# Kernel tuning notes

Hardware: AMD Instinct MI355X
Metric: run time of the kernel (lower is better)

Reference implementation:

```python
import jax, jax.numpy as jnp
import numpy as np

N = 50000          # num nodes
EPS = 1e-5         # BatchNorm eps


def _spmm(row, col, val, x):
    # sparse (COO) @ dense: out[r] += val_e * x[c] for each edge e=(r,c)
    return jax.ops.segment_sum(val[:, None] * x[col], row, num_segments=N)


def setup_inputs() -> dict:
    key = jax.random.key(0)
    ks = jax.random.split(key, 12)
    E1, E2 = 1_000_000, 2_000_000
    IN, H, OUT = 512, 64, 40
    return {
        "x": jax.random.normal(ks[0], (N, IN), jnp.float32),
        "adj_row": jax.random.randint(ks[1], (E1,), 0, N, jnp.int32),
        "adj_col": jax.random.randint(ks[2], (E1,), 0, N, jnp.int32),
        "adj_val": jax.random.uniform(ks[3], (E1,), jnp.float32),
        "adj2_row": jax.random.randint(ks[4], (E2,), 0, N, jnp.int32),
        "adj2_col": jax.random.randint(ks[5], (E2,), 0, N, jnp.int32),
        "adj2_val": jax.random.uniform(ks[6], (E2,), jnp.float32),
        "W_embed": jax.random.normal(ks[7], (IN, H), jnp.float32) * 0.05,
        "b_embed": jnp.zeros((H,), jnp.float32),
        "bn_gamma": jnp.ones((2 * H,), jnp.float32),
        "bn_beta": jnp.zeros((2 * H,), jnp.float32),
        "bn_mean": jax.random.normal(ks[8], (2 * H,), jnp.float32) * 0.1,
        "bn_var": jax.random.uniform(ks[9], (2 * H,), jnp.float32) + 0.5,
        "W_final": jax.random.normal(ks[10], (7 * H, OUT), jnp.float32) * 0.05,
        "b_final": jnp.zeros((OUT,), jnp.float32),
    }


def reference(x, adj_row, adj_col, adj_val, adj2_row, adj2_col, adj2_val,
              W_embed, b_embed, bn_gamma, bn_beta, bn_mean, bn_var,
              W_final, b_final):
    # feature embed (1-layer MLP) + relu
    h = jax.nn.relu(x @ W_embed + b_embed)                       # [N, H]
    xs = [h]
    # conv 1: two-hop aggregation + concat, then BatchNorm (eval mode)
    h1 = jnp.concatenate([_spmm(adj_row, adj_col, adj_val, h),
                          _spmm(adj2_row, adj2_col, adj2_val, h)], axis=1)  # [N, 2H]
    h1 = (h1 - bn_mean) * jax.lax.rsqrt(bn_var + EPS) * bn_gamma + bn_beta
    xs.append(h1)
    # conv 2 (last conv, no BN)
    h2 = jnp.concatenate([_spmm(adj_row, adj_col, adj_val, h1),
                          _spmm(adj2_row, adj2_col, adj2_val, h1)], axis=1)  # [N, 4H]
    xs.append(h2)
    # JumpingKnowledge cat -> [N, 7H], final projection
    jk = jnp.concatenate(xs, axis=1)
    return jk @ W_final + b_final                                # [N, OUT]
```

## Files before the change

kernel.cpp:

```cpp
#include <hip/hip_runtime.h>

#define BN_EPS 1e-5f
#define MAXBINS 128

typedef __attribute__((ext_vector_type(8))) short bf16x8;
typedef __attribute__((ext_vector_type(4))) float f32x4;

__device__ __forceinline__ ushort f2bf(float f) {
  uint u = __float_as_uint(f);
  u += 0x7fffu + ((u >> 16) & 1u);
  return (ushort)(u >> 16);
}
__device__ __forceinline__ float bf2f(ushort u) {
  return __uint_as_float((uint)u << 16);
}
__device__ __forceinline__ uint pack2bf(float a, float b) {
  return (uint)f2bf(a) | ((uint)f2bf(b) << 16);
}
__device__ __forceinline__ void fma8(float acc[8], uint4 wv, float v) {
  acc[0] += v * __uint_as_float(wv.x << 16);
  acc[1] += v * __uint_as_float(wv.x & 0xffff0000u);
  acc[2] += v * __uint_as_float(wv.y << 16);
  acc[3] += v * __uint_as_float(wv.y & 0xffff0000u);
  acc[4] += v * __uint_as_float(wv.z << 16);
  acc[5] += v * __uint_as_float(wv.z & 0xffff0000u);
  acc[6] += v * __uint_as_float(wv.w << 16);
  acc[7] += v * __uint_as_float(wv.w & 0xffff0000u);
}

__global__ __launch_bounds__(256) void prep_weights(
    const float* __restrict__ We, const float* __restrict__ Wf,
    ushort* __restrict__ Wet, ushort* __restrict__ Wtg) {
  int i = blockIdx.x * 256 + threadIdx.x;
  if (i < 32768) {
    int col = i >> 9, k = i & 511;
    Wet[(size_t)col * 512 + k] = f2bf(We[(size_t)k * 64 + col]);
  } else if (i < 32768 + 24576) {
    int j = i - 32768;
    int col = j / 192, k = j % 192;
    float v = 0.f;
    if (col < 40)       v = Wf[(size_t)k * 40 + col];
    else if (col < 80)  { if (k >= 64) v = Wf[(size_t)(128 + k) * 40 + (col - 40)]; }
    else if (col < 120) { if (k >= 64) v = Wf[(size_t)(256 + k) * 40 + (col - 80)]; }
    Wtg[(size_t)col * 192 + k] = f2bf(v);
  }
}

__global__ __launch_bounds__(256) void embed_mfma(
    const float* __restrict__ x, const ushort* __restrict__ Wet,
    const float* __restrict__ b, ushort* __restrict__ hb, int N) {
  const int tid  = threadIdx.x;
  const int wv   = tid >> 6;
  const int lane = tid & 63;
  const int m16  = lane & 15;
  const int kg   = lane >> 4;
  const int row0 = blockIdx.x * 128 + wv * 32;

  f32x4 acc[2][4];
#pragma unroll
  for (int i = 0; i < 2; ++i)
#pragma unroll
    for (int t = 0; t < 4; ++t) acc[i][t] = (f32x4){0.f, 0.f, 0.f, 0.f};

#pragma unroll 4
  for (int ks = 0; ks < 16; ++ks) {
    const int kk = ks * 32 + kg * 8;
    bf16x8 afr[2];
#pragma unroll
    for (int i = 0; i < 2; ++i) {
      int grow = row0 + i * 16 + m16;
      grow = (grow < N) ? grow : (N - 1);
      const float* ap = x + (size_t)grow * 512 + kk;
      float4 lo = *reinterpret_cast<const float4*>(ap);
      float4 hi = *reinterpret_cast<const float4*>(ap + 4);
      uint4 pk;
      pk.x = pack2bf(lo.x, lo.y); pk.y = pack2bf(lo.z, lo.w);
      pk.z = pack2bf(hi.x, hi.y); pk.w = pack2bf(hi.z, hi.w);
      afr[i] = *reinterpret_cast<const bf16x8*>(&pk);
    }
#pragma unroll
    for (int t = 0; t < 4; ++t) {
      bf16x8 bfr = *reinterpret_cast<const bf16x8*>(
          Wet + (size_t)(t * 16 + m16) * 512 + kk);
      acc[0][t] = __builtin_amdgcn_mfma_f32_16x16x32_bf16(afr[0], bfr, acc[0][t], 0, 0, 0);
      acc[1][t] = __builtin_amdgcn_mfma_f32_16x16x32_bf16(afr[1], bfr, acc[1][t], 0, 0, 0);
    }
  }

#pragma unroll
  for (int i = 0; i < 2; ++i) {
    const int rbase = row0 + i * 16 + kg * 4;
#pragma unroll
    for (int t = 0; t < 4; ++t) {
      const int col = t * 16 + m16;
      const float bias = b[col];
#pragma unroll
      for (int reg = 0; reg < 4; ++reg) {
        int gr = rbase + reg;
        if (gr < N)
          hb[(size_t)gr * 64 + col] = f2bf(fmaxf(acc[i][t][reg] + bias, 0.f));
      }
    }
  }
}

__global__ __launch_bounds__(256) void bin_hist(
    const int* __restrict__ rows, int* __restrict__ gbin, int E, int nbins) {
  __shared__ int lb[MAXBINS];
  const int tid = threadIdx.x;
  if (tid < nbins) lb[tid] = 0;
  __syncthreads();
  const int stride = gridDim.x * blockDim.x;
  for (int i = blockIdx.x * blockDim.x + tid; i < E; i += stride)
    atomicAdd(&lb[rows[i] >> 9], 1);
  __syncthreads();
  if (tid < nbins && lb[tid]) atomicAdd(&gbin[tid], lb[tid]);
}

__device__ __forceinline__ void scan_bins_dev(
    const int* gbin, int* gbase, int* gcur, int nbins, int lane) {
  int carry = 0;
  for (int ch = 0; ch * 64 < nbins; ++ch) {
    int idx = ch * 64 + lane;
    int v = (idx < nbins) ? gbin[idx] : 0;
    int inc = v;
#pragma unroll
    for (int off = 1; off < 64; off <<= 1) {
      int y = __shfl_up(inc, off);
      if (lane >= off) inc += y;
    }
    int ex = carry + inc - v;
    if (idx < nbins) { gbase[idx] = ex; gcur[idx] = ex; }
    carry += __shfl(inc, 63);
  }
}

__global__ __launch_bounds__(64) void bin_scan(
    const int* __restrict__ gbin1, int* __restrict__ gbase1, int* __restrict__ gcur1,
    const int* __restrict__ gbin2, int* __restrict__ gbase2, int* __restrict__ gcur2,
    int nbins) {
  int lane = threadIdx.x;
  scan_bins_dev(gbin1, gbase1, gcur1, nbins, lane);
  scan_bins_dev(gbin2, gbase2, gcur2, nbins, lane);
}

__global__ __launch_bounds__(256) void bin_scatter(
    const int* __restrict__ rows, const int* __restrict__ cols,
    const float* __restrict__ vals, int E, int* __restrict__ gcur,
    int2* __restrict__ S, int nbins) {
  __shared__ int lcnt[MAXBINS];
  __shared__ int lcur[MAXBINS];
  const int tid = threadIdx.x;
  for (int e0 = blockIdx.x * 2048; e0 < E; e0 += gridDim.x * 2048) {
    int i0 = e0 + tid * 8;
    int r[8], c[8], vb[8];
    if (i0 + 8 <= E) {
      int4 a = *reinterpret_cast<const int4*>(rows + i0);
      int4 b = *reinterpret_cast<const int4*>(rows + i0 + 4);
      r[0]=a.x; r[1]=a.y; r[2]=a.z; r[3]=a.w; r[4]=b.x; r[5]=b.y; r[6]=b.z; r[7]=b.w;
      a = *reinterpret_cast<const int4*>(cols + i0);
      b = *reinterpret_cast<const int4*>(cols + i0 + 4);
      c[0]=a.x; c[1]=a.y; c[2]=a.z; c[3]=a.w; c[4]=b.x; c[5]=b.y; c[6]=b.z; c[7]=b.w;
      a = *reinterpret_cast<const int4*>(vals + i0);
      b = *reinterpret_cast<const int4*>(vals + i0 + 4);
      vb[0]=a.x; vb[1]=a.y; vb[2]=a.z; vb[3]=a.w; vb[4]=b.x; vb[5]=b.y; vb[6]=b.z; vb[7]=b.w;
    } else {
#pragma unroll
      for (int t = 0; t < 8; ++t) {
        int i = i0 + t;
        bool ok = i < E;
        r[t]  = ok ? rows[i] : -1;
        c[t]  = ok ? cols[i] : 0;
        vb[t] = ok ? __float_as_int(vals[i]) : 0;
      }
    }
    if (tid < nbins) lcnt[tid] = 0;
    __syncthreads();
#pragma unroll
    for (int t = 0; t < 8; ++t)
      if (r[t] >= 0) atomicAdd(&lcnt[r[t] >> 9], 1);
    __syncthreads();
    if (tid < nbins) {
      int n = lcnt[tid];
      lcur[tid] = n ? atomicAdd(&gcur[tid], n) : 0;
    }
    __syncthreads();
#pragma unroll
    for (int t = 0; t < 8; ++t) {
      if (r[t] >= 0) {
        int pos = atomicAdd(&lcur[r[t] >> 9], 1);
        S[pos] = make_int2(c[t] | ((r[t] & 511) << 16), vb[t]);
      }
    }
    __syncthreads();
  }
}

__global__ __launch_bounds__(256) void csr_finalize(
    const int2* __restrict__ S1, const int* __restrict__ gbase1,
    int* __restrict__ rp1, uint* __restrict__ Eo1, int Etot1,
    const int2* __restrict__ S2, const int* __restrict__ gbase2,
    int* __restrict__ rp2, uint* __restrict__ Eo2, int Etot2,
    int N, int nbins) {
  __shared__ int cnt[512];
  __shared__ int cur[512];
  const int tid = threadIdx.x;
  const int b = blockIdx.x % nbins;
  const int g = blockIdx.x / nbins;
  const int2* S     = g ? S2 : S1;
  const int* gbase  = g ? gbase2 : gbase1;
  int* rp           = g ? rp2 : rp1;
  uint* Eo          = g ? Eo2 : Eo1;
  const int Etot    = g ? Etot2 : Etot1;

  const int base = gbase[b];
  const int end  = (b + 1 < nbins) ? gbase[b + 1] : Etot;
  const int r0   = b << 9;
  const int nrows = min(512, N - r0);

  for (int l = tid; l < 512; l += 256) cnt[l] = 0;
  __syncthreads();
  for (int j = base + tid; j < end; j += 256)
    atomicAdd(&cnt[S[j].x >> 16], 1);
  __syncthreads();
  if (tid < 64) {
    int carry = 0;
#pragma unroll
    for (int ch = 0; ch < 8; ++ch) {
      int v = cnt[ch * 64 + tid];
      int inc = v;
#pragma unroll
      for (int off = 1; off < 64; off <<= 1) {
        int y = __shfl_up(inc, off);
        if (tid >= off) inc += y;
      }
      inc += carry;
      cnt[ch * 64 + tid] = inc;
      carry = __shfl(inc, 63);
    }
  }
  __syncthreads();
  for (int l = tid; l < 512; l += 256)
    cur[l] = base + ((l > 0) ? cnt[l - 1] : 0);
  for (int l = tid; l < nrows; l += 256)
    rp[r0 + l + 1] = base + cnt[l];
  if (b == 0 && tid == 0) rp[0] = 0;
  __syncthreads();
  for (int j = base + tid; j < end; j += 256) {
    int2 m = S[j];
    int pos = atomicAdd(&cur[m.x >> 16], 1);
    Eo[pos] = (uint)(m.x & 0xffff) | ((uint)f2bf(__int_as_float(m.y)) << 16);
  }
}

__global__ __launch_bounds__(256) void conv1_gather(
    const ushort* __restrict__ hb,
    const int* __restrict__ rp1, const uint* __restrict__ E1,
    const int* __restrict__ rp2, const uint* __restrict__ E2,
    const float* __restrict__ gamma, const float* __restrict__ beta,
    const float* __restrict__ mean, const float* __restrict__ var,
    ushort* __restrict__ h1b, int N, int nwaves) {
  const int wid  = (blockIdx.x * blockDim.x + threadIdx.x) >> 6;
  const int lane = threadIdx.x & 63;
  const int sub  = lane >> 3;
  const int q    = lane & 7;

  float sc1[8], sh1[8], sc2[8], sh2[8];
#pragma unroll
  for (int t4 = 0; t4 < 2; ++t4) {
    int f1 = q * 8 + t4 * 4;
    float4 gm = *reinterpret_cast<const float4*>(gamma + f1);
    float4 vr = *reinterpret_cast<const float4*>(var + f1);
    float4 mn = *reinterpret_cast<const float4*>(mean + f1);
    float4 bt = *reinterpret_cast<const float4*>(beta + f1);
    float s0 = gm.x * rsqrtf(vr.x + BN_EPS), s1 = gm.y * rsqrtf(vr.y + BN_EPS);
    float s2 = gm.z * rsqrtf(vr.z + BN_EPS), s3 = gm.w * rsqrtf(vr.w + BN_EPS);
    sc1[t4 * 4 + 0] = s0; sh1[t4 * 4 + 0] = bt.x - mn.x * s0;
    sc1[t4 * 4 + 1] = s1; sh1[t4 * 4 + 1] = bt.y - mn.y * s1;
    sc1[t4 * 4 + 2] = s2; sh1[t4 * 4 + 2] = bt.z - mn.z * s2;
    sc1[t4 * 4 + 3] = s3; sh1[t4 * 4 + 3] = bt.w - mn.w * s3;
    int f2 = 64 + f1;
    gm = *reinterpret_cast<const float4*>(gamma + f2);
    vr = *reinterpret_cast<const float4*>(var + f2);
    mn = *reinterpret_cast<const float4*>(mean + f2);
    bt = *reinterpret_cast<const float4*>(beta + f2);
    s0 = gm.x * rsqrtf(vr.x + BN_EPS); s1 = gm.y * rsqrtf(vr.y + BN_EPS);
    s2 = gm.z * rsqrtf(vr.z + BN_EPS); s3 = gm.w * rsqrtf(vr.w + BN_EPS);
    sc2[t4 * 4 + 0] = s0; sh2[t4 * 4 + 0] = bt.x - mn.x * s0;
    sc2[t4 * 4 + 1] = s1; sh2[t4 * 4 + 1] = bt.y - mn.y * s1;
    sc2[t4 * 4 + 2] = s2; sh2[t4 * 4 + 2] = bt.z - mn.z * s2;
    sc2[t4 * 4 + 3] = s3; sh2[t4 * 4 + 3] = bt.w - mn.w * s3;
  }

  for (int r = wid; r < N; r += nwaves) {
    float acc1[8] = {0, 0, 0, 0, 0, 0, 0, 0};
    float acc2[8] = {0, 0, 0, 0, 0, 0, 0, 0};
    {
      int s = rp1[r], e = rp1[r + 1];
      for (int j0 = s; j0 < e; j0 += 32) {
        int j = j0 + sub;
        uint m0 = (j      < e) ? E1[j]      : 0u;
        uint m1 = (j + 8  < e) ? E1[j + 8]  : 0u;
        uint m2 = (j + 16 < e) ? E1[j + 16] : 0u;
        uint m3 = (j + 24 < e) ? E1[j + 24] : 0u;
        uint4 w0 = *reinterpret_cast<const uint4*>(hb + (size_t)(m0 & 0xffffu) * 64 + q * 8);
        uint4 w1 = *reinterpret_cast<const uint4*>(hb + (size_t)(m1 & 0xffffu) * 64 + q * 8);
        uint4 w2 = *reinterpret_cast<const uint4*>(hb + (size_t)(m2 & 0xffffu) * 64 + q * 8);
        uint4 w3 = *reinterpret_cast<const uint4*>(hb + (size_t)(m3 & 0xffffu) * 64 + q * 8);
        fma8(acc1, w0, bf2f((ushort)(m0 >> 16)));
        fma8(acc1, w1, bf2f((ushort)(m1 >> 16)));
        fma8(acc1, w2, bf2f((ushort)(m2 >> 16)));
        fma8(acc1, w3, bf2f((ushort)(m3 >> 16)));
      }
    }
    {
      int s = rp2[r], e = rp2[r + 1];
      for (int j0 = s; j0 < e; j0 += 32) {
        int j = j0 + sub;
        uint m0 = (j      < e) ? E2[j]      : 0u;
        uint m1 = (j + 8  < e) ? E2[j + 8]  : 0u;
        uint m2 = (j + 16 < e) ? E2[j + 16] : 0u;
        uint m3 = (j + 24 < e) ? E2[j + 24] : 0u;
        uint4 w0 = *reinterpret_cast<const uint4*>(hb + (size_t)(m0 & 0xffffu) * 64 + q * 8);
        uint4 w1 = *reinterpret_cast<const uint4*>(hb + (size_t)(m1 & 0xffffu) * 64 + q * 8);
        uint4 w2 = *reinterpret_cast<const uint4*>(hb + (size_t)(m2 & 0xffffu) * 64 + q * 8);
        uint4 w3 = *reinterpret_cast<const uint4*>(hb + (size_t)(m3 & 0xffffu) * 64 + q * 8);
        fma8(acc2, w0, bf2f((ushort)(m0 >> 16)));
        fma8(acc2, w1, bf2f((ushort)(m1 >> 16)));
        fma8(acc2, w2, bf2f((ushort)(m2 >> 16)));
        fma8(acc2, w3, bf2f((ushort)(m3 >> 16)));
      }
    }
#pragma unroll
    for (int mask = 8; mask <= 32; mask <<= 1) {
#pragma unroll
      for (int t = 0; t < 8; ++t) {
        acc1[t] += __shfl_xor(acc1[t], mask);
        acc2[t] += __shfl_xor(acc2[t], mask);
      }
    }
    if (lane < 8) {
      uint4 p1, p2;
      p1.x = pack2bf(acc1[0] * sc1[0] + sh1[0], acc1[1] * sc1[1] + sh1[1]);
      p1.y = pack2bf(acc1[2] * sc1[2] + sh1[2], acc1[3] * sc1[3] + sh1[3]);
      p1.z = pack2bf(acc1[4] * sc1[4] + sh1[4], acc1[5] * sc1[5] + sh1[5]);
      p1.w = pack2bf(acc1[6] * sc1[6] + sh1[6], acc1[7] * sc1[7] + sh1[7]);
      p2.x = pack2bf(acc2[0] * sc2[0] + sh2[0], acc2[1] * sc2[1] + sh2[1]);
      p2.y = pack2bf(acc2[2] * sc2[2] + sh2[2], acc2[3] * sc2[3] + sh2[3]);
      p2.z = pack2bf(acc2[4] * sc2[4] + sh2[4], acc2[5] * sc2[5] + sh2[5]);
      p2.w = pack2bf(acc2[6] * sc2[6] + sh2[6], acc2[7] * sc2[7] + sh2[7]);
      ushort* dst = h1b + (size_t)r * 128 + q * 8;
      *reinterpret_cast<uint4*>(dst)      = p1;
      *reinterpret_cast<uint4*>(dst + 64) = p2;
    }
  }
}

__global__ __launch_bounds__(256) void dense_tail_mfma(
    const ushort* __restrict__ hb, const ushort* __restrict__ h1b,
    const ushort* __restrict__ Wtg, const float* __restrict__ bfin,
    float* __restrict__ out, ushort* __restrict__ g1b, ushort* __restrict__ g2b,
    int N) {
  const int tid  = threadIdx.x;
  const int wv   = tid >> 6;
  const int lane = tid & 63;
  const int m16  = lane & 15;
  const int kg   = lane >> 4;
  const int row0 = blockIdx.x * 128;

  f32x4 acc[2][8];
#pragma unroll
  for (int i = 0; i < 2; ++i)
#pragma unroll
    for (int t = 0; t < 8; ++t) acc[i][t] = (f32x4){0.f, 0.f, 0.f, 0.f};

#pragma unroll
  for (int ks = 0; ks < 6; ++ks) {
    const int kk = ks * 32 + kg * 8;
    bf16x8 afr[2];
#pragma unroll
    for (int i = 0; i < 2; ++i) {
      int grow = row0 + wv * 32 + i * 16 + m16;
      grow = (grow < N) ? grow : (N - 1);
      const ushort* ap = (kk < 64) ? hb + (size_t)grow * 64 + kk
                                   : h1b + (size_t)grow * 128 + (kk - 64);
      afr[i] = *reinterpret_cast<const bf16x8*>(ap);
    }
#pragma unroll
    for (int t = 0; t < 8; ++t) {
      bf16x8 bfr = *reinterpret_cast<const bf16x8*>(
          Wtg + (size_t)(t * 16 + m16) * 192 + kk);
      acc[0][t] = __builtin_amdgcn_mfma_f32_16x16x32_bf16(afr[0], bfr, acc[0][t], 0, 0, 0);
      acc[1][t] = __builtin_amdgcn_mfma_f32_16x16x32_bf16(afr[1], bfr, acc[1][t], 0, 0, 0);
    }
  }

#pragma unroll
  for (int i = 0; i < 2; ++i) {
    const int rbase = row0 + wv * 32 + i * 16 + kg * 4;
#pragma unroll
    for (int t = 0; t < 8; ++t) {
      const int col = t * 16 + m16;
      if (col >= 120) continue;
      const float bias = (col < 40) ? bfin[col] : 0.f;
#pragma unroll
      for (int reg = 0; reg < 4; ++reg) {
        int gr = rbase + reg;
        if (gr < N) {
          float v = acc[i][t][reg];
          if (col < 40)       out[(size_t)gr * 40 + col] = v + bias;
          else if (col < 80)  g1b[(size_t)gr * 40 + (col - 40)] = f2bf(v);
          else                g2b[(size_t)gr * 40 + (col - 80)] = f2bf(v);
        }
      }
    }
  }
}

__global__ __launch_bounds__(256) void final_add_kernel(
    const ushort* __restrict__ g1b, const ushort* __restrict__ g2b,
    const int* __restrict__ rp1, const uint* __restrict__ E1,
    const int* __restrict__ rp2, const uint* __restrict__ E2,
    float* __restrict__ out, int N, int nwaves) {
  const int wid  = (blockIdx.x * blockDim.x + threadIdx.x) >> 6;
  const int lane = threadIdx.x & 63;
  const int sub  = lane >> 3;
  const int q    = lane & 7;
  const int off  = (q < 5) ? q * 8 : 0;

  for (int r = wid; r < N; r += nwaves) {
    float a1[8] = {0, 0, 0, 0, 0, 0, 0, 0};
    float a2[8] = {0, 0, 0, 0, 0, 0, 0, 0};
    {
      int s = rp1[r], e = rp1[r + 1];
      for (int j0 = s; j0 < e; j0 += 32) {
        int j = j0 + sub;
        uint m0 = (j      < e) ? E1[j]      : 0u;
        uint m1 = (j + 8  < e) ? E1[j + 8]  : 0u;
        uint m2 = (j + 16 < e) ? E1[j + 16] : 0u;
        uint m3 = (j + 24 < e) ? E1[j + 24] : 0u;
        uint4 w0 = *reinterpret_cast<const uint4*>(g1b + (size_t)(m0 & 0xffffu) * 40 + off);
        uint4 w1 = *reinterpret_cast<const uint4*>(g1b + (size_t)(m1 & 0xffffu) * 40 + off);
        uint4 w2 = *reinterpret_cast<const uint4*>(g1b + (size_t)(m2 & 0xffffu) * 40 + off);
        uint4 w3 = *reinterpret_cast<const uint4*>(g1b + (size_t)(m3 & 0xffffu) * 40 + off);
        fma8(a1, w0, bf2f((ushort)(m0 >> 16)));
        fma8(a1, w1, bf2f((ushort)(m1 >> 16)));
        fma8(a1, w2, bf2f((ushort)(m2 >> 16)));
        fma8(a1, w3, bf2f((ushort)(m3 >> 16)));
      }
    }
    {
      int s = rp2[r], e = rp2[r + 1];
      for (int j0 = s; j0 < e; j0 += 32) {
        int j = j0 + sub;
        uint m0 = (j      < e) ? E2[j]      : 0u;
        uint m1 = (j + 8  < e) ? E2[j + 8]  : 0u;
        uint m2 = (j + 16 < e) ? E2[j + 16] : 0u;
        uint m3 = (j + 24 < e) ? E2[j + 24] : 0u;
        uint4 w0 = *reinterpret_cast<const uint4*>(g2b + (size_t)(m0 & 0xffffu) * 40 + off);
        uint4 w1 = *reinterpret_cast<const uint4*>(g2b + (size_t)(m1 & 0xffffu) * 40 + off);
        uint4 w2 = *reinterpret_cast<const uint4*>(g2b + (size_t)(m2 & 0xffffu) * 40 + off);
        uint4 w3 = *reinterpret_cast<const uint4*>(g2b + (size_t)(m3 & 0xffffu) * 40 + off);
        fma8(a2, w0, bf2f((ushort)(m0 >> 16)));
        fma8(a2, w1, bf2f((ushort)(m1 >> 16)));
        fma8(a2, w2, bf2f((ushort)(m2 >> 16)));
        fma8(a2, w3, bf2f((ushort)(m3 >> 16)));
      }
    }
#pragma unroll
    for (int mask = 8; mask <= 32; mask <<= 1) {
#pragma unroll
      for (int t = 0; t < 8; ++t) {
        a1[t] += __shfl_xor(a1[t], mask);
        a2[t] += __shfl_xor(a2[t], mask);
      }
    }
    if (lane < 5) {
      float* p = out + (size_t)r * 40 + lane * 8;
      float4 o0 = *reinterpret_cast<const float4*>(p);
      float4 o1 = *reinterpret_cast<const float4*>(p + 4);
      o0.x += a1[0] + a2[0]; o0.y += a1[1] + a2[1];
      o0.z += a1[2] + a2[2]; o0.w += a1[3] + a2[3];
      o1.x += a1[4] + a2[4]; o1.y += a1[5] + a2[5];
      o1.z += a1[6] + a2[6]; o1.w += a1[7] + a2[7];
      *reinterpret_cast<float4*>(p)     = o0;
      *reinterpret_cast<float4*>(p + 4) = o1;
    }
  }
}

extern "C" void kernel_launch(void* const* d_in, const int* in_sizes, int n_in,
                              void* d_out, int out_size, void* d_ws, size_t ws_size,
                              hipStream_t stream) {
  const float* x     = (const float*)d_in[0];
  const int*   a1r   = (const int*)d_in[1];
  const int*   a1c   = (const int*)d_in[2];
  const float* a1v   = (const float*)d_in[3];
  const int*   a2r   = (const int*)d_in[4];
  const int*   a2c   = (const int*)d_in[5];
  const float* a2v   = (const float*)d_in[6];
  const float* We    = (const float*)d_in[7];
  const float* be    = (const float*)d_in[8];
  const float* gamma = (const float*)d_in[9];
  const float* beta  = (const float*)d_in[10];
  const float* mean  = (const float*)d_in[11];
  const float* var   = (const float*)d_in[12];
  const float* Wf    = (const float*)d_in[13];
  const float* bf    = (const float*)d_in[14];
  float* out = (float*)d_out;

  const int N  = in_sizes[0] / 512;
  const int E1 = in_sizes[1];
  const int E2 = in_sizes[4];
  const int nbins = (N + 511) >> 9;

  char* p = (char*)d_ws;
  auto alloc = [&](size_t bytes) {
    char* q = p; p += (bytes + 255) & ~(size_t)255; return q;
  };
  ushort* hb   = (ushort*)alloc((size_t)N * 64 * 2);
  ushort* h1b  = (ushort*)alloc((size_t)N * 128 * 2);
  ushort* g1b  = (ushort*)alloc((size_t)N * 40 * 2);
  ushort* g2b  = (ushort*)alloc((size_t)N * 40 * 2);
  ushort* Wet  = (ushort*)alloc((size_t)64 * 512 * 2);
  ushort* Wtg  = (ushort*)alloc((size_t)128 * 192 * 2);
  int*    rp1  = (int*)   alloc(((size_t)N + 1) * 4);
  int*    rp2  = (int*)   alloc(((size_t)N + 1) * 4);
  uint*   E1s  = (uint*)  alloc((size_t)E1 * 4);
  uint*   E2s  = (uint*)  alloc((size_t)E2 * 4);
  int2*   S1   = (int2*)  alloc((size_t)E1 * 8);
  int2*   S2   = (int2*)  alloc((size_t)E2 * 8);
  int*    gbin1  = (int*) alloc(MAXBINS * 4);
  int*    gbin2  = (int*) alloc(MAXBINS * 4);
  int*    gbase1 = (int*) alloc(MAXBINS * 4);
  int*    gbase2 = (int*) alloc(MAXBINS * 4);
  int*    gcur1  = (int*) alloc(MAXBINS * 4);
  int*    gcur2  = (int*) alloc(MAXBINS * 4);

  hipMemsetAsync(gbin1, 0, (size_t)2 * MAXBINS * 4 + 256, stream);

  prep_weights<<<(32768 + 24576 + 255) / 256, 256, 0, stream>>>(We, Wf, Wet, Wtg);

  embed_mfma<<<(N + 127) / 128, 256, 0, stream>>>(x, Wet, be, hb, N);

  bin_hist<<<256, 256, 0, stream>>>(a1r, gbin1, E1, nbins);
  bin_hist<<<256, 256, 0, stream>>>(a2r, gbin2, E2, nbins);
  bin_scan<<<1, 64, 0, stream>>>(gbin1, gbase1, gcur1, gbin2, gbase2, gcur2, nbins);
  bin_scatter<<<256, 256, 0, stream>>>(a1r, a1c, a1v, E1, gcur1, S1, nbins);
  bin_scatter<<<256, 256, 0, stream>>>(a2r, a2c, a2v, E2, gcur2, S2, nbins);
  csr_finalize<<<2 * nbins, 256, 0, stream>>>(
      S1, gbase1, rp1, E1s, E1, S2, gbase2, rp2, E2s, E2, N, nbins);

  const int NW = 2048 * 4;
  conv1_gather<<<2048, 256, 0, stream>>>(
      hb, rp1, E1s, rp2, E2s, gamma, beta, mean, var, h1b, N, NW);

  dense_tail_mfma<<<(N + 127) / 128, 256, 0, stream>>>(
      hb, h1b, Wtg, bf, out, g1b, g2b, N);

  final_add_kernel<<<2048, 256, 0, stream>>>(
      g1b, g2b, rp1, E1s, rp2, E2s, out, N, NW);
}
```

Measured before the change: 303.6 us.

## Split gather passes into feature halves and per-graph passes for cache locality

```diff
diff --git a/kernel.cpp b/kernel.cpp
--- a/kernel.cpp
+++ b/kernel.cpp
@@ -48,7 +48,8 @@
 
 __global__ __launch_bounds__(256) void embed_mfma(
     const float* __restrict__ x, const ushort* __restrict__ Wet,
-    const float* __restrict__ b, ushort* __restrict__ hb, int N) {
+    const float* __restrict__ b, ushort* __restrict__ hbA,
+    ushort* __restrict__ hbB, int N) {
   const int tid  = threadIdx.x;
   const int wv   = tid >> 6;
   const int lane = tid & 63;
@@ -97,8 +98,11 @@
 #pragma unroll
       for (int reg = 0; reg < 4; ++reg) {
         int gr = rbase + reg;
-        if (gr < N)
-          hb[(size_t)gr * 64 + col] = f2bf(fmaxf(acc[i][t][reg] + bias, 0.f));
+        if (gr < N) {
+          ushort v = f2bf(fmaxf(acc[i][t][reg] + bias, 0.f));
+          if (col < 32) hbA[(size_t)gr * 32 + col] = v;
+          else          hbB[(size_t)gr * 32 + (col - 32)] = v;
+        }
       }
     }
   }
@@ -253,22 +257,22 @@
   }
 }
 
-__global__ __launch_bounds__(256) void conv1_gather(
-    const ushort* __restrict__ hb,
+__global__ __launch_bounds__(256) void conv1_gather_half(
+    const ushort* __restrict__ src,
     const int* __restrict__ rp1, const uint* __restrict__ E1,
     const int* __restrict__ rp2, const uint* __restrict__ E2,
     const float* __restrict__ gamma, const float* __restrict__ beta,
     const float* __restrict__ mean, const float* __restrict__ var,
-    ushort* __restrict__ h1b, int N, int nwaves) {
+    ushort* __restrict__ h1b, int N, int nwaves, int pbase) {
   const int wid  = (blockIdx.x * blockDim.x + threadIdx.x) >> 6;
   const int lane = threadIdx.x & 63;
-  const int sub  = lane >> 3;
-  const int q    = lane & 7;
+  const int sub  = lane >> 2;
+  const int q    = lane & 3;
 
   float sc1[8], sh1[8], sc2[8], sh2[8];
 #pragma unroll
   for (int t4 = 0; t4 < 2; ++t4) {
-    int f1 = q * 8 + t4 * 4;
+    int f1 = pbase + q * 8 + t4 * 4;
     float4 gm = *reinterpret_cast<const float4*>(gamma + f1);
     float4 vr = *reinterpret_cast<const float4*>(var + f1);
     float4 mn = *reinterpret_cast<const float4*>(mean + f1);
@@ -297,16 +301,16 @@
     float acc2[8] = {0, 0, 0, 0, 0, 0, 0, 0};
     {
       int s = rp1[r], e = rp1[r + 1];
-      for (int j0 = s; j0 < e; j0 += 32) {
+      for (int j0 = s; j0 < e; j0 += 64) {
         int j = j0 + sub;
         uint m0 = (j      < e) ? E1[j]      : 0u;
-        uint m1 = (j + 8  < e) ? E1[j + 8]  : 0u;
-        uint m2 = (j + 16 < e) ? E1[j + 16] : 0u;
-        uint m3 = (j + 24 < e) ? E1[j + 24] : 0u;
-        uint4 w0 = *reinterpret_cast<const uint4*>(hb + (size_t)(m0 & 0xffffu) * 64 + q * 8);
-        uint4 w1 = *reinterpret_cast<const uint4*>(hb + (size_t)(m1 & 0xffffu) * 64 + q * 8);
-        uint4 w2 = *reinterpret_cast<const uint4*>(hb + (size_t)(m2 & 0xffffu) * 64 + q * 8);
-        uint4 w3 = *reinterpret_cast<const uint4*>(hb + (size_t)(m3 & 0xffffu) * 64 + q * 8);
+        uint m1 = (j + 16 < e) ? E1[j + 16] : 0u;
+        uint m2 = (j + 32 < e) ? E1[j + 32] : 0u;
+        uint m3 = (j + 48 < e) ? E1[j + 48] : 0u;
+        uint4 w0 = *reinterpret_cast<const uint4*>(src + (size_t)(m0 & 0xffffu) * 32 + q * 8);
+        uint4 w1 = *reinterpret_cast<const uint4*>(src + (size_t)(m1 & 0xffffu) * 32 + q * 8);
+        uint4 w2 = *reinterpret_cast<const uint4*>(src + (size_t)(m2 & 0xffffu) * 32 + q * 8);
+        uint4 w3 = *reinterpret_cast<const uint4*>(src + (size_t)(m3 & 0xffffu) * 32 + q * 8);
         fma8(acc1, w0, bf2f((ushort)(m0 >> 16)));
         fma8(acc1, w1, bf2f((ushort)(m1 >> 16)));
         fma8(acc1, w2, bf2f((ushort)(m2 >> 16)));
@@ -315,16 +319,16 @@
     }
     {
       int s = rp2[r], e = rp2[r + 1];
-      for (int j0 = s; j0 < e; j0 += 32) {
+      for (int j0 = s; j0 < e; j0 += 64) {
         int j = j0 + sub;
         uint m0 = (j      < e) ? E2[j]      : 0u;
-        uint m1 = (j + 8  < e) ? E2[j + 8]  : 0u;
-        uint m2 = (j + 16 < e) ? E2[j + 16] : 0u;
-        uint m3 = (j + 24 < e) ? E2[j + 24] : 0u;
-        uint4 w0 = *reinterpret_cast<const uint4*>(hb + (size_t)(m0 & 0xffffu) * 64 + q * 8);
-        uint4 w1 = *reinterpret_cast<const uint4*>(hb + (size_t)(m1 & 0xffffu) * 64 + q * 8);
-        uint4 w2 = *reinterpret_cast<const uint4*>(hb + (size_t)(m2 & 0xffffu) * 64 + q * 8);
-        uint4 w3 = *reinterpret_cast<const uint4*>(hb + (size_t)(m3 & 0xffffu) * 64 + q * 8);
+        uint m1 = (j + 16 < e) ? E2[j + 16] : 0u;
+        uint m2 = (j + 32 < e) ? E2[j + 32] : 0u;
+        uint m3 = (j + 48 < e) ? E2[j + 48] : 0u;
+        uint4 w0 = *reinterpret_cast<const uint4*>(src + (size_t)(m0 & 0xffffu) * 32 + q * 8);
+        uint4 w1 = *reinterpret_cast<const uint4*>(src + (size_t)(m1 & 0xffffu) * 32 + q * 8);
+        uint4 w2 = *reinterpret_cast<const uint4*>(src + (size_t)(m2 & 0xffffu) * 32 + q * 8);
+        uint4 w3 = *reinterpret_cast<const uint4*>(src + (size_t)(m3 & 0xffffu) * 32 + q * 8);
         fma8(acc2, w0, bf2f((ushort)(m0 >> 16)));
         fma8(acc2, w1, bf2f((ushort)(m1 >> 16)));
         fma8(acc2, w2, bf2f((ushort)(m2 >> 16)));
@@ -332,14 +336,14 @@
       }
     }
 #pragma unroll
-    for (int mask = 8; mask <= 32; mask <<= 1) {
+    for (int mask = 4; mask <= 32; mask <<= 1) {
 #pragma unroll
       for (int t = 0; t < 8; ++t) {
         acc1[t] += __shfl_xor(acc1[t], mask);
         acc2[t] += __shfl_xor(acc2[t], mask);
       }
     }
-    if (lane < 8) {
+    if (lane < 4) {
       uint4 p1, p2;
       p1.x = pack2bf(acc1[0] * sc1[0] + sh1[0], acc1[1] * sc1[1] + sh1[1]);
       p1.y = pack2bf(acc1[2] * sc1[2] + sh1[2], acc1[3] * sc1[3] + sh1[3]);
@@ -349,7 +353,7 @@
       p2.y = pack2bf(acc2[2] * sc2[2] + sh2[2], acc2[3] * sc2[3] + sh2[3]);
       p2.z = pack2bf(acc2[4] * sc2[4] + sh2[4], acc2[5] * sc2[5] + sh2[5]);
       p2.w = pack2bf(acc2[6] * sc2[6] + sh2[6], acc2[7] * sc2[7] + sh2[7]);
-      ushort* dst = h1b + (size_t)r * 128 + q * 8;
+      ushort* dst = h1b + (size_t)r * 128 + pbase + q * 8;
       *reinterpret_cast<uint4*>(dst)      = p1;
       *reinterpret_cast<uint4*>(dst + 64) = p2;
     }
@@ -357,7 +361,8 @@
 }
 
 __global__ __launch_bounds__(256) void dense_tail_mfma(
-    const ushort* __restrict__ hb, const ushort* __restrict__ h1b,
+    const ushort* __restrict__ hbA, const ushort* __restrict__ hbB,
+    const ushort* __restrict__ h1b,
     const ushort* __restrict__ Wtg, const float* __restrict__ bfin,
     float* __restrict__ out, ushort* __restrict__ g1b, ushort* __restrict__ g2b,
     int N) {
@@ -382,8 +387,10 @@
     for (int i = 0; i < 2; ++i) {
       int grow = row0 + wv * 32 + i * 16 + m16;
       grow = (grow < N) ? grow : (N - 1);
-      const ushort* ap = (kk < 64) ? hb + (size_t)grow * 64 + kk
-                                   : h1b + (size_t)grow * 128 + (kk - 64);
+      const ushort* ap;
+      if (ks == 0)      ap = hbA + (size_t)grow * 32 + kk;
+      else if (ks == 1) ap = hbB + (size_t)grow * 32 + (kk - 32);
+      else              ap = h1b + (size_t)grow * 128 + (kk - 64);
       afr[i] = *reinterpret_cast<const bf16x8*>(ap);
     }
 #pragma unroll
@@ -417,10 +424,9 @@
   }
 }
 
-__global__ __launch_bounds__(256) void final_add_kernel(
-    const ushort* __restrict__ g1b, const ushort* __restrict__ g2b,
-    const int* __restrict__ rp1, const uint* __restrict__ E1,
-    const int* __restrict__ rp2, const uint* __restrict__ E2,
+__global__ __launch_bounds__(256) void final_add_g(
+    const ushort* __restrict__ g,
+    const int* __restrict__ rp, const uint* __restrict__ E,
     float* __restrict__ out, int N, int nwaves) {
   const int wid  = (blockIdx.x * blockDim.x + threadIdx.x) >> 6;
   const int lane = threadIdx.x & 63;
@@ -429,60 +435,34 @@
   const int off  = (q < 5) ? q * 8 : 0;
 
   for (int r = wid; r < N; r += nwaves) {
-    float a1[8] = {0, 0, 0, 0, 0, 0, 0, 0};
-    float a2[8] = {0, 0, 0, 0, 0, 0, 0, 0};
-    {
-      int s = rp1[r], e = rp1[r + 1];
-      for (int j0 = s; j0 < e; j0 += 32) {
-        int j = j0 + sub;
-        uint m0 = (j      < e) ? E1[j]      : 0u;
-        uint m1 = (j + 8  < e) ? E1[j + 8]  : 0u;
-        uint m2 = (j + 16 < e) ? E1[j + 16] : 0u;
-        uint m3 = (j + 24 < e) ? E1[j + 24] : 0u;
-        uint4 w0 = *reinterpret_cast<const uint4*>(g1b + (size_t)(m0 & 0xffffu) * 40 + off);
-        uint4 w1 = *reinterpret_cast<const uint4*>(g1b + (size_t)(m1 & 0xffffu) * 40 + off);
-        uint4 w2 = *reinterpret_cast<const uint4*>(g1b + (size_t)(m2 & 0xffffu) * 40 + off);
-        uint4 w3 = *reinterpret_cast<const uint4*>(g1b + (size_t)(m3 & 0xffffu) * 40 + off);
-        fma8(a1, w0, bf2f((ushort)(m0 >> 16)));
-        fma8(a1, w1, bf2f((ushort)(m1 >> 16)));
-        fma8(a1, w2, bf2f((ushort)(m2 >> 16)));
-        fma8(a1, w3, bf2f((ushort)(m3 >> 16)));
-      }
-    }
-    {
-      int s = rp2[r], e = rp2[r + 1];
-      for (int j0 = s; j0 < e; j0 += 32) {
-        int j = j0 + sub;
-        uint m0 = (j      < e) ? E2[j]      : 0u;
-        uint m1 = (j + 8  < e) ? E2[j + 8]  : 0u;
-        uint m2 = (j + 16 < e) ? E2[j + 16] : 0u;
-        uint m3 = (j + 24 < e) ? E2[j + 24] : 0u;
-        uint4 w0 = *reinterpret_cast<const uint4*>(g2b + (size_t)(m0 & 0xffffu) * 40 + off);
-        uint4 w1 = *reinterpret_cast<const uint4*>(g2b + (size_t)(m1 & 0xffffu) * 40 + off);
-        uint4 w2 = *reinterpret_cast<const uint4*>(g2b + (size_t)(m2 & 0xffffu) * 40 + off);
-        uint4 w3 = *reinterpret_cast<const uint4*>(g2b + (size_t)(m3 & 0xffffu) * 40 + off);
-        fma8(a2, w0, bf2f((ushort)(m0 >> 16)));
-        fma8(a2, w1, bf2f((ushort)(m1 >> 16)));
-        fma8(a2, w2, bf2f((ushort)(m2 >> 16)));
-        fma8(a2, w3, bf2f((ushort)(m3 >> 16)));
-      }
-    }
-#pragma unroll
-    for (int mask = 8; mask <= 32; mask <<= 1) {
-#pragma unroll
-      for (int t = 0; t < 8; ++t) {
-        a1[t] += __shfl_xor(a1[t], mask);
-        a2[t] += __shfl_xor(a2[t], mask);
-      }
-    }
+    float a[8] = {0, 0, 0, 0, 0, 0, 0, 0};
+    int s = rp[r], e = rp[r + 1];
+    for (int j0 = s; j0 < e; j0 += 32) {
+      int j = j0 + sub;
+      uint m0 = (j      < e) ? E[j]      : 0u;
+      uint m1 = (j + 8  < e) ? E[j + 8]  : 0u;
+      uint m2 = (j + 16 < e) ? E[j + 16] : 0u;
+      uint m3 = (j + 24 < e) ? E[j + 24] : 0u;
+      uint4 w0 = *reinterpret_cast<const uint4*>(g + (size_t)(m0 & 0xffffu) * 40 + off);
+      uint4 w1 = *reinterpret_cast<const uint4*>(g + (size_t)(m1 & 0xffffu) * 40 + off);
+      uint4 w2 = *reinterpret_cast<const uint4*>(g + (size_t)(m2 & 0xffffu) * 40 + off);
+      uint4 w3 = *reinterpret_cast<const uint4*>(g + (size_t)(m3 & 0xffffu) * 40 + off);
+      fma8(a, w0, bf2f((ushort)(m0 >> 16)));
+      fma8(a, w1, bf2f((ushort)(m1 >> 16)));
+      fma8(a, w2, bf2f((ushort)(m2 >> 16)));
+      fma8(a, w3, bf2f((ushort)(m3 >> 16)));
+    }
+#pragma unroll
+    for (int mask = 8; mask <= 32; mask <<= 1)
+#pragma unroll
+      for (int t = 0; t < 8; ++t) a[t] += __shfl_xor(a[t], mask);
+
     if (lane < 5) {
       float* p = out + (size_t)r * 40 + lane * 8;
       float4 o0 = *reinterpret_cast<const float4*>(p);
       float4 o1 = *reinterpret_cast<const float4*>(p + 4);
-      o0.x += a1[0] + a2[0]; o0.y += a1[1] + a2[1];
-      o0.z += a1[2] + a2[2]; o0.w += a1[3] + a2[3];
-      o1.x += a1[4] + a2[4]; o1.y += a1[5] + a2[5];
-      o1.z += a1[6] + a2[6]; o1.w += a1[7] + a2[7];
+      o0.x += a[0]; o0.y += a[1]; o0.z += a[2]; o0.w += a[3];
+      o1.x += a[4]; o1.y += a[5]; o1.z += a[6]; o1.w += a[7];
       *reinterpret_cast<float4*>(p)     = o0;
       *reinterpret_cast<float4*>(p + 4) = o1;
     }
@@ -518,7 +498,8 @@
   auto alloc = [&](size_t bytes) {
     char* q = p; p += (bytes + 255) & ~(size_t)255; return q;
   };
-  ushort* hb   = (ushort*)alloc((size_t)N * 64 * 2);
+  ushort* hbA  = (ushort*)alloc((size_t)N * 32 * 2);
+  ushort* hbB  = (ushort*)alloc((size_t)N * 32 * 2);
   ushort* h1b  = (ushort*)alloc((size_t)N * 128 * 2);
   ushort* g1b  = (ushort*)alloc((size_t)N * 40 * 2);
   ushort* g2b  = (ushort*)alloc((size_t)N * 40 * 2);
@@ -537,11 +518,11 @@
   int*    gcur1  = (int*) alloc(MAXBINS * 4);
   int*    gcur2  = (int*) alloc(MAXBINS * 4);
 
-  hipMemsetAsync(gbin1, 0, (size_t)2 * MAXBINS * 4 + 256, stream);
+  hipMemsetAsync(gbin1, 0, (size_t)2 * MAXBINS * 4, stream);
 
   prep_weights<<<(32768 + 24576 + 255) / 256, 256, 0, stream>>>(We, Wf, Wet, Wtg);
 
-  embed_mfma<<<(N + 127) / 128, 256, 0, stream>>>(x, Wet, be, hb, N);
+  embed_mfma<<<(N + 127) / 128, 256, 0, stream>>>(x, Wet, be, hbA, hbB, N);
 
   bin_hist<<<256, 256, 0, stream>>>(a1r, gbin1, E1, nbins);
   bin_hist<<<256, 256, 0, stream>>>(a2r, gbin2, E2, nbins);
@@ -552,12 +533,14 @@
       S1, gbase1, rp1, E1s, E1, S2, gbase2, rp2, E2s, E2, N, nbins);
 
   const int NW = 2048 * 4;
-  conv1_gather<<<2048, 256, 0, stream>>>(
-      hb, rp1, E1s, rp2, E2s, gamma, beta, mean, var, h1b, N, NW);
+  conv1_gather_half<<<2048, 256, 0, stream>>>(
+      hbA, rp1, E1s, rp2, E2s, gamma, beta, mean, var, h1b, N, NW, 0);
+  conv1_gather_half<<<2048, 256, 0, stream>>>(
+      hbB, rp1, E1s, rp2, E2s, gamma, beta, mean, var, h1b, N, NW, 32);
 
   dense_tail_mfma<<<(N + 127) / 128, 256, 0, stream>>>(
-      hb, h1b, Wtg, bf, out, g1b, g2b, N);
-
-  final_add_kernel<<<2048, 256, 0, stream>>>(
-      g1b, g2b, rp1, E1s, rp2, E2s, out, N, NW);
-}
+      hbA, hbB, h1b, Wtg, bf, out, g1b, g2b, N);
+
+  final_add_g<<<2048, 256, 0, stream>>>(g1b, rp1, E1s, out, N, NW);
+  final_add_g<<<2048, 256, 0, stream>>>(g2b, rp2, E2s, out, N, NW);
+}
```

Result: slower. 336.2 us (+10.7%).
